# Kernel optimization log

Measured on AMD Instinct MI355X. Metric: run time of the kernel, lower is better.

The kernel has to match this reference:

```python
import jax, jax.numpy as jnp
import numpy as np

SEQ_LEN, BATCH = 1024, 256
VOCAB, EMBED, HIDDEN = 32000, 512, 1024


def setup_inputs() -> dict:
    key = jax.random.key(0)
    k1, k2, k3, k4, k5, k6 = jax.random.split(key, 6)
    return {
        "x_seq": jax.random.randint(k1, (SEQ_LEN, BATCH), 0, VOCAB, dtype=jnp.int64)
        if jax.config.jax_enable_x64 else jax.random.randint(k1, (SEQ_LEN, BATCH), 0, VOCAB, dtype=jnp.int32),
        "emb": jax.random.normal(k2, (VOCAB, EMBED), dtype=jnp.float32) * 0.02,
        "W_ih": jax.random.normal(k3, (HIDDEN, EMBED), dtype=jnp.float32) * 0.02,
        "b_ih": jax.random.normal(k4, (HIDDEN,), dtype=jnp.float32) * 0.02,
        "W_hh": jax.random.normal(k5, (HIDDEN, HIDDEN), dtype=jnp.float32) * 0.02,
        "b_hh": jax.random.normal(k6, (HIDDEN,), dtype=jnp.float32) * 0.02,
    }


def reference(x_seq, emb, W_ih, b_ih, W_hh, b_hh):
    # x_seq: [S, B] int -> embedded: [S, B, E]
    embedded = emb[x_seq]
    # Input projection is time-independent: batch it into one big GEMM
    # (same math as per-step W_ih(x_t) + bias in the torch loop).
    x_proj = jnp.einsum("sbe,he->sbh", embedded, W_ih) + b_ih  # [S, B, H]

    h0 = jnp.zeros((x_seq.shape[1], W_hh.shape[0]), dtype=emb.dtype)

    def step(h, xp_t):
        # h_{t} = tanh(W_ih x_t + b_ih + W_hh h_{t-1} + b_hh)
        h_new = jnp.tanh(xp_t + h @ W_hh.T + b_hh)
        return h_new, h_new

    _, hidden_states = jax.lax.scan(step, h0, x_proj)  # [S, B, H]
    return hidden_states
```

## Files before the change

### kernel.cpp

```cpp
#include <hip/hip_runtime.h>
#include <hip/hip_bf16.h>

typedef unsigned short u16;
typedef unsigned int u32;
typedef __attribute__((ext_vector_type(8))) short short8v;
typedef __attribute__((ext_vector_type(8))) unsigned short ushort8v;
typedef __attribute__((ext_vector_type(4))) float float4v;
typedef __attribute__((ext_vector_type(4))) unsigned int uint4v;
typedef __attribute__((ext_vector_type(2))) unsigned int uint2v;

#define S_LEN 1024
#define BATCH 256
#define VOCAB 32000
#define EMBED 512
#define HIDDEN 1024
#define BH (BATCH * HIDDEN)
#define FLAG_STRIDE 32

__device__ inline u16 f2bf(float f) {
  return __builtin_bit_cast(u16, __float2bfloat16(f));
}

__device__ inline short8v cohload16(const u16* base, int voff) {
  __amdgpu_buffer_rsrc_t r =
      __builtin_amdgcn_make_buffer_rsrc((void*)base, (short)0, -1, 0x00020000);
  uint4v d = __builtin_amdgcn_raw_buffer_load_b128(r, voff, 0, 17);
  return __builtin_bit_cast(short8v, d);
}
__device__ inline void cohstore8(u16* base, int voff, uint2v v) {
  __amdgpu_buffer_rsrc_t r =
      __builtin_amdgcn_make_buffer_rsrc((void*)base, (short)0, -1, 0x00020000);
  __builtin_amdgcn_raw_buffer_store_b64(v, r, voff, 0, 17);
}

__device__ inline short8v cvt8(float4v a, float4v b) {
  ushort8v v;
  v[0]=f2bf(a[0]); v[1]=f2bf(a[1]); v[2]=f2bf(a[2]); v[3]=f2bf(a[3]);
  v[4]=f2bf(b[0]); v[5]=f2bf(b[1]); v[6]=f2bf(b[2]); v[7]=f2bf(b[3]);
  return __builtin_bit_cast(short8v, v);
}

__global__ __launch_bounds__(256) void prep_kernel(u16* __restrict__ ws16,
                                                   const float* __restrict__ emb,
                                                   u16* __restrict__ emb16,
                                                   int do_emb) {
  int i = blockIdx.x * 256 + threadIdx.x;
  const int NZ = 73728;
  if (i < NZ) {
    ushort8v z = {0,0,0,0,0,0,0,0};
    *(ushort8v*)(ws16 + (size_t)i * 8) = z;
  } else if (do_emb) {
    int j = i - NZ;
    if (j < (VOCAB * EMBED) / 8) {
      const float* s = emb + (size_t)j * 8;
      *(ushort8v*)(emb16 + (size_t)j * 8) = __builtin_bit_cast(
          ushort8v, cvt8(*(const float4v*)s, *(const float4v*)(s + 4)));
    }
  }
}

__global__ __launch_bounds__(256, 1) void rnn_fused(const int* __restrict__ xseq,
                                                    const float* __restrict__ emb,
                                                    const float* __restrict__ wih,
                                                    const float* __restrict__ bih,
                                                    const float* __restrict__ whh,
                                                    const float* __restrict__ bhh,
                                                    u16* __restrict__ hbuf,
                                                    float* __restrict__ out,
                                                    u32* __restrict__ flag,
                                                    const u16* __restrict__ emb16,
                                                    int eb16) {
  extern __shared__ u16 smem[];
  u16* xq = smem;
  float (*red)[4][16][68] = (float (*)[4][16][68])(smem + S_LEN * 16);
  const int tid = threadIdx.x;
  const int lane = tid & 63, w = tid >> 6;
  const int l15 = lane & 15, l4 = lane >> 4;
  const int g = blockIdx.x & 15;
  const int jt = blockIdx.x >> 4;

  short8v Wf[4][8];
  #pragma unroll
  for (int jj = 0; jj < 4; jj++)
    #pragma unroll
    for (int kq = 0; kq < 8; kq++) {
      const float* s = whh + (size_t)(jt * 64 + jj * 16 + l15) * HIDDEN
                       + w * 256 + kq * 32 + l4 * 8;
      Wf[jj][kq] = cvt8(*(const float4v*)s, *(const float4v*)(s + 4));
    }
  short8v Wihf[4][4];
  #pragma unroll
  for (int jj = 0; jj < 4; jj++)
    #pragma unroll
    for (int kk = 0; kk < 4; kk++) {
      const float* s = wih + (size_t)(jt * 64 + jj * 16 + l15) * EMBED
                       + w * 128 + kk * 32 + l4 * 8;
      Wihf[jj][kk] = cvt8(*(const float4v*)s, *(const float4v*)(s + 4));
    }
  for (int i = tid; i < S_LEN * 16; i += 256)
    xq[i] = (u16)xseq[(i >> 4) * BATCH + g * 16 + (i & 15)];
  const int trow = w * 4 + (lane >> 4);
  const int tc4 = (lane & 15) * 4;
  float bsum[4];
  #pragma unroll
  for (int i = 0; i < 4; i++)
    bsum[i] = bhh[jt * 64 + tc4 + i] + bih[jt * 64 + tc4 + i];
  const int aoff = ((g * 16 + l15) * HIDDEN + w * 256 + l4 * 8) * 2;
  const int hoff = ((g * 16 + trow) * HIDDEN + jt * 64 + tc4) * 2;
  __syncthreads();

  float4v xacc[4] = {};
  if (eb16) {
    const u16* er0 = emb16 + (size_t)xq[l15] * EMBED + w * 128 + l4 * 8;
    #pragma unroll
    for (int kk = 0; kk < 4; kk++) {
      short8v af = *(const short8v*)(er0 + kk * 32);
      #pragma unroll
      for (int jj = 0; jj < 4; jj++)
        xacc[jj] = __builtin_amdgcn_mfma_f32_16x16x32_bf16(af, Wihf[jj][kk], xacc[jj], 0, 0, 0);
    }
  } else {
    const float* er0 = emb + (size_t)xq[l15] * EMBED + w * 128 + l4 * 8;
    #pragma unroll
    for (int kk = 0; kk < 4; kk++) {
      short8v af = cvt8(*(const float4v*)(er0 + kk * 32),
                        *(const float4v*)(er0 + kk * 32 + 4));
      #pragma unroll
      for (int jj = 0; jj < 4; jj++)
        xacc[jj] = __builtin_amdgcn_mfma_f32_16x16x32_bf16(af, Wihf[jj][kk], xacc[jj], 0, 0, 0);
    }
  }

  for (int t = 0; t < S_LEN; t++) {
    const int p = t & 1;
    float* outt = out + (size_t)t * BH;
    float4v accp[4] = {xacc[0], xacc[1], xacc[2], xacc[3]};
    if (t > 0) {
      if (lane < 16) {
        const u32* f = flag +
            ((size_t)(g * 16 + w * 4 + (lane >> 2)) * 4 + (lane & 3)) * FLAG_STRIDE;
        while (__hip_atomic_load(f, __ATOMIC_RELAXED, __HIP_MEMORY_SCOPE_AGENT) < (u32)t) { }
      }
    }
    __builtin_amdgcn_sched_barrier(0);
    const u16* hp = hbuf + (size_t)p * BH;
    short8v a[8];
    #pragma unroll
    for (int kq = 0; kq < 8; kq++)
      a[kq] = cohload16(hp, aoff + kq * 64);
    __builtin_amdgcn_sched_barrier(0);
    int tn = (t + 1 < S_LEN) ? (t + 1) : t;
    short8v ebf[4];
    float4v e[8];
    if (eb16) {
      const u16* er = emb16 + (size_t)xq[tn * 16 + l15] * EMBED + w * 128 + l4 * 8;
      #pragma unroll
      for (int kk = 0; kk < 4; kk++)
        ebf[kk] = *(const short8v*)(er + kk * 32);
    } else {
      const float* er = emb + (size_t)xq[tn * 16 + l15] * EMBED + w * 128 + l4 * 8;
      #pragma unroll
      for (int kk = 0; kk < 4; kk++) {
        e[2 * kk]     = *(const float4v*)(er + kk * 32);
        e[2 * kk + 1] = *(const float4v*)(er + kk * 32 + 4);
      }
    }
    #pragma unroll
    for (int kq = 0; kq < 8; kq++)
      #pragma unroll
      for (int jj = 0; jj < 4; jj++)
        accp[jj] = __builtin_amdgcn_mfma_f32_16x16x32_bf16(a[kq], Wf[jj][kq], accp[jj], 0, 0, 0);
    #pragma unroll
    for (int jj = 0; jj < 4; jj++)
      #pragma unroll
      for (int q = 0; q < 4; q++)
        red[p][w][l4 * 4 + q][jj * 16 + l15] = accp[jj][q];
    __syncthreads();
    float4v r0 = *(const float4v*)&red[p][0][trow][tc4];
    float4v r1 = *(const float4v*)&red[p][1][trow][tc4];
    float4v r2 = *(const float4v*)&red[p][2][trow][tc4];
    float4v r3 = *(const float4v*)&red[p][3][trow][tc4];
    float th[4];
    #pragma unroll
    for (int i = 0; i < 4; i++) {
      float s = r0[i] + r1[i] + r2[i] + r3[i] + bsum[i];
      float ex = __expf(-2.0f * fabsf(s));
      float v = (1.0f - ex) / (1.0f + ex);
      th[i] = copysignf(v, s);
    }
    uint2v hv;
    hv[0] = (u32)f2bf(th[0]) | ((u32)f2bf(th[1]) << 16);
    hv[1] = (u32)f2bf(th[2]) | ((u32)f2bf(th[3]) << 16);
    u16* hq = hbuf + (size_t)(p ^ 1) * BH;
    cohstore8(hq, hoff, hv);
    asm volatile("s_waitcnt vmcnt(0)" ::: "memory");
    if (lane == 0)
      __hip_atomic_store(flag + ((size_t)(g * 16 + jt) * 4 + w) * FLAG_STRIDE,
                         (u32)(t + 1), __ATOMIC_RELAXED, __HIP_MEMORY_SCOPE_AGENT);
    float4v o = {th[0], th[1], th[2], th[3]};
    *(float4v*)(outt + (size_t)(g * 16 + trow) * HIDDEN + jt * 64 + tc4) = o;
    float4v xn[4] = {};
    #pragma unroll
    for (int kk = 0; kk < 4; kk++) {
      short8v af = eb16 ? ebf[kk] : cvt8(e[2 * kk], e[2 * kk + 1]);
      #pragma unroll
      for (int jj = 0; jj < 4; jj++)
        xn[jj] = __builtin_amdgcn_mfma_f32_16x16x32_bf16(af, Wihf[jj][kk], xn[jj], 0, 0, 0);
    }
    xacc[0] = xn[0]; xacc[1] = xn[1]; xacc[2] = xn[2]; xacc[3] = xn[3];
  }
}

extern "C" void kernel_launch(void* const* d_in, const int* in_sizes, int n_in,
                              void* d_out, int out_size, void* d_ws, size_t ws_size,
                              hipStream_t stream) {
  const int* xseq   = (const int*)d_in[0];
  const float* emb  = (const float*)d_in[1];
  const float* wih  = (const float*)d_in[2];
  const float* bih  = (const float*)d_in[3];
  const float* whh  = (const float*)d_in[4];
  const float* bhh  = (const float*)d_in[5];
  float* out = (float*)d_out;
  char* ws = (char*)d_ws;
  u16* hbuf  = (u16*)ws;
  u32* flag  = (u32*)(ws + 1048576);
  u16* emb16 = (u16*)(ws + 1179648);

  const size_t need = 1179648u + (size_t)VOCAB * EMBED * 2u;
  const int do_emb = (ws_size >= need) ? 1 : 0;
  const int prep_items = 73728 + (do_emb ? (VOCAB * EMBED) / 8 : 0);

  prep_kernel<<<(prep_items + 255) / 256, 256, 0, stream>>>((u16*)ws, emb, emb16, do_emb);
  (void)hipFuncSetAttribute((const void*)rnn_fused,
                            hipFuncAttributeMaxDynamicSharedMemorySize, 67584);
  rnn_fused<<<256, 256, 67584, stream>>>(xseq, emb, wih, bih, whh, bhh,
                                         hbuf, out, flag, emb16, do_emb);
}
```

Baseline: 3.359 ms.

## Replace flag polling with sequence-tagged hidden-state messages in swizzled mailbox layout

Removes the separate per-block flag array and the store-wait-flag handshake. Each thread now writes a 16-byte message holding the step counter plus four bf16 hidden values into a mailbox laid out so each consumer lane reads its MFMA A-fragment directly. Consumers spin on the 16 loads until every tag matches the step. This cuts the store-drain-then-flag latency on the critical path, but doubles the bytes moved per step because of the tag padding. It relies on 16-byte stores being observed atomically across blocks.

```diff
diff --git a/kernel.cpp b/kernel.cpp
--- a/kernel.cpp
+++ b/kernel.cpp
@@ -7,7 +7,6 @@
 typedef __attribute__((ext_vector_type(8))) unsigned short ushort8v;
 typedef __attribute__((ext_vector_type(4))) float float4v;
 typedef __attribute__((ext_vector_type(4))) unsigned int uint4v;
-typedef __attribute__((ext_vector_type(2))) unsigned int uint2v;
 
 #define S_LEN 1024
 #define BATCH 256
@@ -15,22 +14,16 @@
 #define EMBED 512
 #define HIDDEN 1024
 #define BH (BATCH * HIDDEN)
-#define FLAG_STRIDE 32
+#define MB_SLOT 1048576
 
 __device__ inline u16 f2bf(float f) {
   return __builtin_bit_cast(u16, __float2bfloat16(f));
 }
 
-__device__ inline short8v cohload16(const u16* base, int voff) {
+__device__ inline void cohstore16u(u16* base, int voff, uint4v v) {
   __amdgpu_buffer_rsrc_t r =
       __builtin_amdgcn_make_buffer_rsrc((void*)base, (short)0, -1, 0x00020000);
-  uint4v d = __builtin_amdgcn_raw_buffer_load_b128(r, voff, 0, 17);
-  return __builtin_bit_cast(short8v, d);
-}
-__device__ inline void cohstore8(u16* base, int voff, uint2v v) {
-  __amdgpu_buffer_rsrc_t r =
-      __builtin_amdgcn_make_buffer_rsrc((void*)base, (short)0, -1, 0x00020000);
-  __builtin_amdgcn_raw_buffer_store_b64(v, r, voff, 0, 17);
+  __builtin_amdgcn_raw_buffer_store_b128(v, r, voff, 0, 17);
 }
 
 __device__ inline short8v cvt8(float4v a, float4v b) {
@@ -40,15 +33,20 @@
   return __builtin_bit_cast(short8v, v);
 }
 
-__global__ __launch_bounds__(256) void prep_kernel(u16* __restrict__ ws16,
+__device__ inline short8v mkfrag(uint4v A, uint4v B) {
+  uint4v f = {A[1], A[2], B[1], B[2]};
+  return __builtin_bit_cast(short8v, f);
+}
+
+__global__ __launch_bounds__(256) void prep_kernel(u16* __restrict__ mbx,
                                                    const float* __restrict__ emb,
                                                    u16* __restrict__ emb16,
                                                    int do_emb) {
   int i = blockIdx.x * 256 + threadIdx.x;
-  const int NZ = 73728;
+  const int NZ = (2 * MB_SLOT) / 16;
   if (i < NZ) {
     ushort8v z = {0,0,0,0,0,0,0,0};
-    *(ushort8v*)(ws16 + (size_t)i * 8) = z;
+    *(ushort8v*)(mbx + (size_t)i * 8) = z;
   } else if (do_emb) {
     int j = i - NZ;
     if (j < (VOCAB * EMBED) / 8) {
@@ -65,9 +63,8 @@
                                                     const float* __restrict__ bih,
                                                     const float* __restrict__ whh,
                                                     const float* __restrict__ bhh,
-                                                    u16* __restrict__ hbuf,
+                                                    u16* __restrict__ mbx,
                                                     float* __restrict__ out,
-                                                    u32* __restrict__ flag,
                                                     const u16* __restrict__ emb16,
                                                     int eb16) {
   extern __shared__ u16 smem[];
@@ -105,8 +102,11 @@
   #pragma unroll
   for (int i = 0; i < 4; i++)
     bsum[i] = bhh[jt * 64 + tc4 + i] + bih[jt * 64 + tc4 + i];
-  const int aoff = ((g * 16 + l15) * HIDDEN + w * 256 + l4 * 8) * 2;
-  const int hoff = ((g * 16 + trow) * HIDDEN + jt * 64 + tc4) * 2;
+  const int w_t = jt >> 2;
+  const int l_t = trow + 16 * ((tc4 >> 3) & 3);
+  const int u_idx = (jt & 3) * 4 + ((tc4 >> 5) & 1) * 2 + ((tc4 >> 2) & 1);
+  const int moff = (((g * 4 + w_t) * 64 + l_t) * 16 + u_idx) * 16;
+  const int cbase = ((g * 4 + w) * 64 + lane) * 128;
   __syncthreads();
 
   float4v xacc[4] = {};
@@ -132,23 +132,8 @@
   }
 
   for (int t = 0; t < S_LEN; t++) {
-    const int p = t & 1;
     float* outt = out + (size_t)t * BH;
     float4v accp[4] = {xacc[0], xacc[1], xacc[2], xacc[3]};
-    if (t > 0) {
-      if (lane < 16) {
-        const u32* f = flag +
-            ((size_t)(g * 16 + w * 4 + (lane >> 2)) * 4 + (lane & 3)) * FLAG_STRIDE;
-        while (__hip_atomic_load(f, __ATOMIC_RELAXED, __HIP_MEMORY_SCOPE_AGENT) < (u32)t) { }
-      }
-    }
-    __builtin_amdgcn_sched_barrier(0);
-    const u16* hp = hbuf + (size_t)p * BH;
-    short8v a[8];
-    #pragma unroll
-    for (int kq = 0; kq < 8; kq++)
-      a[kq] = cohload16(hp, aoff + kq * 64);
-    __builtin_amdgcn_sched_barrier(0);
     int tn = (t + 1 < S_LEN) ? (t + 1) : t;
     short8v ebf[4];
     float4v e[8];
@@ -165,11 +150,52 @@
         e[2 * kk + 1] = *(const float4v*)(er + kk * 32 + 4);
       }
     }
-    #pragma unroll
-    for (int kq = 0; kq < 8; kq++)
-      #pragma unroll
-      for (int jj = 0; jj < 4; jj++)
-        accp[jj] = __builtin_amdgcn_mfma_f32_16x16x32_bf16(a[kq], Wf[jj][kq], accp[jj], 0, 0, 0);
+    if (t > 0) {
+      const u16* pb = mbx + (size_t)(t & 1) * (MB_SLOT / 2) + cbase;
+      uint4v u0,u1,u2,u3,u4,u5,u6,u7,u8,u9,u10,u11,u12,u13,u14,u15;
+      const u32 tt = (u32)t;
+      bool ok;
+      do {
+        asm volatile(
+          "global_load_dwordx4 %0, %16, off sc0 sc1\n\t"
+          "global_load_dwordx4 %1, %16, off offset:16 sc0 sc1\n\t"
+          "global_load_dwordx4 %2, %16, off offset:32 sc0 sc1\n\t"
+          "global_load_dwordx4 %3, %16, off offset:48 sc0 sc1\n\t"
+          "global_load_dwordx4 %4, %16, off offset:64 sc0 sc1\n\t"
+          "global_load_dwordx4 %5, %16, off offset:80 sc0 sc1\n\t"
+          "global_load_dwordx4 %6, %16, off offset:96 sc0 sc1\n\t"
+          "global_load_dwordx4 %7, %16, off offset:112 sc0 sc1\n\t"
+          "global_load_dwordx4 %8, %16, off offset:128 sc0 sc1\n\t"
+          "global_load_dwordx4 %9, %16, off offset:144 sc0 sc1\n\t"
+          "global_load_dwordx4 %10, %16, off offset:160 sc0 sc1\n\t"
+          "global_load_dwordx4 %11, %16, off offset:176 sc0 sc1\n\t"
+          "global_load_dwordx4 %12, %16, off offset:192 sc0 sc1\n\t"
+          "global_load_dwordx4 %13, %16, off offset:208 sc0 sc1\n\t"
+          "global_load_dwordx4 %14, %16, off offset:224 sc0 sc1\n\t"
+          "global_load_dwordx4 %15, %16, off offset:240 sc0 sc1\n\t"
+          "s_waitcnt vmcnt(0)"
+          : "=&v"(u0), "=&v"(u1), "=&v"(u2), "=&v"(u3),
+            "=&v"(u4), "=&v"(u5), "=&v"(u6), "=&v"(u7),
+            "=&v"(u8), "=&v"(u9), "=&v"(u10), "=&v"(u11),
+            "=&v"(u12), "=&v"(u13), "=&v"(u14), "=&v"(u15)
+          : "v"(pb) : "memory");
+        ok = (u0[0]==tt) & (u1[0]==tt) & (u2[0]==tt) & (u3[0]==tt) &
+             (u4[0]==tt) & (u5[0]==tt) & (u6[0]==tt) & (u7[0]==tt) &
+             (u8[0]==tt) & (u9[0]==tt) & (u10[0]==tt) & (u11[0]==tt) &
+             (u12[0]==tt) & (u13[0]==tt) & (u14[0]==tt) & (u15[0]==tt);
+      } while (!ok);
+      short8v afr[8];
+      afr[0] = mkfrag(u0, u1);   afr[1] = mkfrag(u2, u3);
+      afr[2] = mkfrag(u4, u5);   afr[3] = mkfrag(u6, u7);
+      afr[4] = mkfrag(u8, u9);   afr[5] = mkfrag(u10, u11);
+      afr[6] = mkfrag(u12, u13); afr[7] = mkfrag(u14, u15);
+      #pragma unroll
+      for (int kq = 0; kq < 8; kq++)
+        #pragma unroll
+        for (int jj = 0; jj < 4; jj++)
+          accp[jj] = __builtin_amdgcn_mfma_f32_16x16x32_bf16(afr[kq], Wf[jj][kq], accp[jj], 0, 0, 0);
+    }
+    const int p = t & 1;
     #pragma unroll
     for (int jj = 0; jj < 4; jj++)
       #pragma unroll
@@ -188,15 +214,12 @@
       float v = (1.0f - ex) / (1.0f + ex);
       th[i] = copysignf(v, s);
     }
-    uint2v hv;
-    hv[0] = (u32)f2bf(th[0]) | ((u32)f2bf(th[1]) << 16);
-    hv[1] = (u32)f2bf(th[2]) | ((u32)f2bf(th[3]) << 16);
-    u16* hq = hbuf + (size_t)(p ^ 1) * BH;
-    cohstore8(hq, hoff, hv);
-    asm volatile("s_waitcnt vmcnt(0)" ::: "memory");
-    if (lane == 0)
-      __hip_atomic_store(flag + ((size_t)(g * 16 + jt) * 4 + w) * FLAG_STRIDE,
-                         (u32)(t + 1), __ATOMIC_RELAXED, __HIP_MEMORY_SCOPE_AGENT);
+    uint4v mval;
+    mval[0] = (u32)(t + 1);
+    mval[1] = (u32)f2bf(th[0]) | ((u32)f2bf(th[1]) << 16);
+    mval[2] = (u32)f2bf(th[2]) | ((u32)f2bf(th[3]) << 16);
+    mval[3] = 0u;
+    cohstore16u(mbx, ((t + 1) & 1) * MB_SLOT + moff, mval);
     float4v o = {th[0], th[1], th[2], th[3]};
     *(float4v*)(outt + (size_t)(g * 16 + trow) * HIDDEN + jt * 64 + tc4) = o;
     float4v xn[4] = {};
@@ -222,17 +245,16 @@
   const float* bhh  = (const float*)d_in[5];
   float* out = (float*)d_out;
   char* ws = (char*)d_ws;
-  u16* hbuf  = (u16*)ws;
-  u32* flag  = (u32*)(ws + 1048576);
-  u16* emb16 = (u16*)(ws + 1179648);
-
-  const size_t need = 1179648u + (size_t)VOCAB * EMBED * 2u;
+  u16* mbx   = (u16*)ws;
+  u16* emb16 = (u16*)(ws + 2097152);
+
+  const size_t need = 2097152u + (size_t)VOCAB * EMBED * 2u;
   const int do_emb = (ws_size >= need) ? 1 : 0;
-  const int prep_items = 73728 + (do_emb ? (VOCAB * EMBED) / 8 : 0);
-
-  prep_kernel<<<(prep_items + 255) / 256, 256, 0, stream>>>((u16*)ws, emb, emb16, do_emb);
+  const int prep_items = 131072 + (do_emb ? (VOCAB * EMBED) / 8 : 0);
+
+  prep_kernel<<<(prep_items + 255) / 256, 256, 0, stream>>>(mbx, emb, emb16, do_emb);
   (void)hipFuncSetAttribute((const void*)rnn_fused,
                             hipFuncAttributeMaxDynamicSharedMemorySize, 67584);
   rnn_fused<<<256, 256, 67584, stream>>>(xseq, emb, wih, bih, whh, bhh,
-                                         hbuf, out, flag, emb16, do_emb);
-}
+                                         mbx, out, emb16, do_emb);
+}
```

After: 5.587 ms. +66.3%, slower.
